# Optimization experiments

Hardware: AMD Instinct MI355X
Metric: run time of the kernel (lower is better)

Reference implementation:

```python
import jax, jax.numpy as jnp
import numpy as np

DIM = 512
HEADS = 4
HEAD_DIM = DIM // HEADS
HIDDEN = DIM * 2
DEPTH = 4
N = 32768
T = 4  # fixed branch/token dim


def _layernorm(x, w, b, eps=1e-5):
    m = jnp.mean(x, axis=-1, keepdims=True)
    v = jnp.mean(jnp.square(x - m), axis=-1, keepdims=True)
    return (x - m) * jax.lax.rsqrt(v + eps) * w + b


def setup_inputs() -> dict:
    key = jax.random.key(0)
    ks = jax.random.split(key, 24)
    s = 0.02
    d = {
        'x': jax.random.normal(ks[0], (N, DIM, T), dtype=jnp.float32),
        'branch_embed': s * jax.random.normal(ks[1], (T, DIM), dtype=jnp.float32),
        'ln1_w': jnp.ones((DEPTH, DIM), jnp.float32),
        'ln1_b': jnp.zeros((DEPTH, DIM), jnp.float32),
        'qkv_w': s * jax.random.normal(ks[2], (DEPTH, 3 * DIM, DIM), dtype=jnp.float32),
        'qkv_b': jnp.zeros((DEPTH, 3 * DIM), jnp.float32),
        'proj_w': s * jax.random.normal(ks[3], (DEPTH, DIM, DIM), dtype=jnp.float32),
        'proj_b': jnp.zeros((DEPTH, DIM), jnp.float32),
        'ln2_w': jnp.ones((DEPTH, DIM), jnp.float32),
        'ln2_b': jnp.zeros((DEPTH, DIM), jnp.float32),
        'ffn_w1': s * jax.random.normal(ks[4], (DEPTH, HIDDEN, DIM), dtype=jnp.float32),
        'ffn_b1': jnp.zeros((DEPTH, HIDDEN), jnp.float32),
        'ffn_w2': s * jax.random.normal(ks[5], (DEPTH, DIM, HIDDEN), dtype=jnp.float32),
        'ffn_b2': jnp.zeros((DEPTH, DIM), jnp.float32),
        'pool_q': s * jax.random.normal(ks[6], (DIM,), dtype=jnp.float32),
        'pool_w': s * jax.random.normal(ks[7], (DIM, DIM), dtype=jnp.float32),
        'out_ln_w': jnp.ones((DIM,), jnp.float32),
        'out_ln_b': jnp.zeros((DIM,), jnp.float32),
        'out_w1': s * jax.random.normal(ks[8], (DIM // 2, DIM), dtype=jnp.float32),
        'out_b1': jnp.zeros((DIM // 2,), jnp.float32),
        'out_w2': s * jax.random.normal(ks[9], (1, DIM // 2), dtype=jnp.float32),
        'out_b2': jnp.zeros((1,), jnp.float32),
    }
    return d


def reference(x, branch_embed, ln1_w, ln1_b, qkv_w, qkv_b, proj_w, proj_b,
              ln2_w, ln2_b, ffn_w1, ffn_b1, ffn_w2, ffn_b2,
              pool_q, pool_w, out_ln_w, out_ln_b, out_w1, out_b1, out_w2, out_b2):
    # (N, C, 4) -> (N, 4, C), add branch embedding
    x = jnp.swapaxes(x, 1, 2) + branch_embed[None]
    n = x.shape[0]
    scale = 1.0 / np.sqrt(HEAD_DIM)
    for i in range(DEPTH):
        # --- MHSA (pre-LN, eval mode -> dropout off) ---
        h = _layernorm(x, ln1_w[i], ln1_b[i])
        qkv = jnp.einsum('ntd,ed->nte', h, qkv_w[i]) + qkv_b[i]  # (N, T, 3D)
        q, k, v = jnp.split(qkv, 3, axis=-1)
        q = q.reshape(n, T, HEADS, HEAD_DIM).transpose(0, 2, 1, 3)
        k = k.reshape(n, T, HEADS, HEAD_DIM).transpose(0, 2, 1, 3)
        v = v.reshape(n, T, HEADS, HEAD_DIM).transpose(0, 2, 1, 3)
        scores = jnp.einsum('nhqd,nhkd->nhqk', q, k) * scale
        attn = jax.nn.softmax(scores, axis=-1)
        o = jnp.einsum('nhqk,nhkd->nhqd', attn, v)
        o = o.transpose(0, 2, 1, 3).reshape(n, T, DIM)
        o = jnp.einsum('ntd,ed->nte', o, proj_w[i]) + proj_b[i]
        x = x + o
        # --- FFN ---
        h = _layernorm(x, ln2_w[i], ln2_b[i])
        f = jax.nn.gelu(jnp.einsum('ntd,hd->nth', h, ffn_w1[i]) + ffn_b1[i], approximate=False)
        f = jnp.einsum('nth,dh->ntd', f, ffn_w2[i]) + ffn_b2[i]
        x = x + f
    # --- attention pooling head ---
    k = jnp.einsum('ntd,ed->nte', x, pool_w)            # pool_proj (no bias)
    score = jax.nn.softmax(jnp.einsum('d,ntd->nt', pool_q, k) / np.sqrt(DIM), axis=-1)
    z = jnp.einsum('nt,ntd->nd', score, x)
    z = _layernorm(z, out_ln_w, out_ln_b)
    z = jax.nn.gelu(z @ out_w1.T + out_b1, approximate=False)
    y = (z @ out_w2.T + out_b2)[:, 0]
    return y
```

## Files before the change

kernel.cpp:

```cpp
#include <hip/hip_runtime.h>

typedef unsigned short u16;
typedef unsigned int u32;
typedef __attribute__((ext_vector_type(8))) short s16x8;
typedef __attribute__((ext_vector_type(8))) unsigned short u16x8;
typedef __attribute__((ext_vector_type(4))) float f32x4;

__device__ __forceinline__ u16 f2bf(float f) {
    u32 u = __float_as_uint(f);
    u32 r = (u + 0x7fffu + ((u >> 16) & 1u)) >> 16;
    return (u16)r;
}
__device__ __forceinline__ float bf2f(u16 u) { return __uint_as_float(((u32)u) << 16); }
__device__ __forceinline__ float bflo(u32 u) { return __uint_as_float(u << 16); }
__device__ __forceinline__ float bfhi(u32 u) { return __uint_as_float(u & 0xffff0000u); }
__device__ __forceinline__ float gelu_exact(float v) {
    return 0.5f * v * (1.0f + erff(v * 0.70710678118654752f));
}

__device__ __forceinline__ void gload16(const void* g, void* l) {
    __builtin_amdgcn_global_load_lds(
        (const __attribute__((address_space(1))) u32*)g,
        (__attribute__((address_space(3))) u32*)l, 16, 0, 0);
}

__global__ void k_cvt(const float* __restrict__ in, u16* __restrict__ out, int n4) {
    int i = blockIdx.x * 256 + threadIdx.x;
    if (i < n4) {
        float4 v = *(const float4*)(in + (size_t)i * 4);
        u16 o0 = f2bf(v.x), o1 = f2bf(v.y), o2 = f2bf(v.z), o3 = f2bf(v.w);
        u32 lo = (u32)o0 | ((u32)o1 << 16);
        u32 hi = (u32)o2 | ((u32)o3 << 16);
        uint2 o; o.x = lo; o.y = hi;
        *(uint2*)(out + (size_t)i * 4) = o;
    }
}

__global__ __launch_bounds__(256) void k_embed_ln(const float* __restrict__ x,
                                                  const float* __restrict__ be,
                                                  const float* __restrict__ w,
                                                  const float* __restrict__ b,
                                                  u16* __restrict__ Xb,
                                                  u16* __restrict__ Hb) {
    __shared__ u16 ld[4][512];
    int s = blockIdx.x;
    int tid = threadIdx.x;
    const float* xs = x + (size_t)s * 2048;
#pragma unroll
    for (int i = 0; i < 2; ++i) {
        int d = tid + i * 256;
        float4 v = *(const float4*)(xs + d * 4);
        ld[0][d] = f2bf(v.x + be[d]);
        ld[1][d] = f2bf(v.y + be[512 + d]);
        ld[2][d] = f2bf(v.z + be[1024 + d]);
        ld[3][d] = f2bf(v.w + be[1536 + d]);
    }
    __syncthreads();
    int t = tid >> 6, lane = tid & 63;
    u16x8 raw = *(const u16x8*)(&ld[t][lane * 8]);
    *(u16x8*)(Xb + ((size_t)s * 4 + t) * 512 + lane * 8) = raw;
    float a[8];
#pragma unroll
    for (int j = 0; j < 8; ++j) a[j] = bf2f(raw[j]);
    float s1 = 0.f, s2 = 0.f;
#pragma unroll
    for (int j = 0; j < 8; ++j) { s1 += a[j]; s2 += a[j] * a[j]; }
#pragma unroll
    for (int d = 1; d < 64; d <<= 1) { s1 += __shfl_xor(s1, d); s2 += __shfl_xor(s2, d); }
    float mean = s1 * (1.0f / 512.0f);
    float var  = s2 * (1.0f / 512.0f) - mean * mean;
    float rstd = rsqrtf(var + 1e-5f);
    float4 w0 = *(const float4*)(w + lane * 8);
    float4 w1 = *(const float4*)(w + lane * 8 + 4);
    float4 b0 = *(const float4*)(b + lane * 8);
    float4 b1 = *(const float4*)(b + lane * 8 + 4);
    float wv[8] = {w0.x, w0.y, w0.z, w0.w, w1.x, w1.y, w1.z, w1.w};
    float bv[8] = {b0.x, b0.y, b0.z, b0.w, b1.x, b1.y, b1.z, b1.w};
    u16x8 o;
#pragma unroll
    for (int j = 0; j < 8; ++j) o[j] = f2bf((a[j] - mean) * rstd * wv[j] + bv[j]);
    *(u16x8*)(Hb + ((size_t)s * 4 + t) * 512 + lane * 8) = o;
}

__global__ __launch_bounds__(256) void k_ln(const u16* __restrict__ Xb,
                                            const float* __restrict__ w,
                                            const float* __restrict__ b,
                                            u16* __restrict__ H) {
    int row = blockIdx.x * 4 + (threadIdx.x >> 6);
    int lane = threadIdx.x & 63;
    u16x8 xv = *(const u16x8*)(Xb + (size_t)row * 512 + lane * 8);
    float a[8];
#pragma unroll
    for (int j = 0; j < 8; ++j) a[j] = bf2f(xv[j]);
    float s1 = 0.f, s2 = 0.f;
#pragma unroll
    for (int j = 0; j < 8; ++j) { s1 += a[j]; s2 += a[j] * a[j]; }
#pragma unroll
    for (int d = 1; d < 64; d <<= 1) { s1 += __shfl_xor(s1, d); s2 += __shfl_xor(s2, d); }
    float mean = s1 * (1.0f / 512.0f);
    float var  = s2 * (1.0f / 512.0f) - mean * mean;
    float rstd = rsqrtf(var + 1e-5f);
    float4 w0 = *(const float4*)(w + lane * 8);
    float4 w1 = *(const float4*)(w + lane * 8 + 4);
    float4 b0 = *(const float4*)(b + lane * 8);
    float4 b1 = *(const float4*)(b + lane * 8 + 4);
    float wv[8] = {w0.x, w0.y, w0.z, w0.w, w1.x, w1.y, w1.z, w1.w};
    float bv[8] = {b0.x, b0.y, b0.z, b0.w, b1.x, b1.y, b1.z, b1.w};
    u16x8 o;
#pragma unroll
    for (int j = 0; j < 8; ++j) o[j] = f2bf((a[j] - mean) * rstd * wv[j] + bv[j]);
    *(u16x8*)(H + (size_t)row * 512 + lane * 8) = o;
}

template <bool BIAS, bool GELU_, bool RESID>
__global__ __launch_bounds__(512, 2) void k_gemm256(const u16* __restrict__ A,
                                                    const u16* __restrict__ W,
                                                    const float* __restrict__ bias,
                                                    u16* __restrict__ Cb,
                                                    u16* __restrict__ Xbres,
                                                    int K, int ncols, int TN, int T) {
    __shared__ __align__(16) u16 lds[2 * 32768];
    int tid = threadIdx.x;
    int lane = tid & 63;
    int wid = tid >> 6;
    int G = gridDim.x, b = blockIdx.x;
    int start, end, step;
    if ((G & 7) == 0) {
        int xcd = b & 7, nxb = G >> 3, j = b >> 3;
        start = (int)(((long long)xcd * T) >> 3) + j;
        end   = (int)(((long long)(xcd + 1) * T) >> 3);
        step  = nxb;
    } else {
        start = (int)(((long long)b * T) / G);
        end   = (int)(((long long)(b + 1) * T) / G);
        step  = 1;
    }
    if (start >= end) return;
    int NS = K >> 6;
    int mgrp = wid >> 2, ngrp = wid & 3;

    f32x4 acc[8][4];
#pragma unroll
    for (int i = 0; i < 8; ++i)
#pragma unroll
        for (int j = 0; j < 4; ++j) acc[i][j] = (f32x4){0.f, 0.f, 0.f, 0.f};

    int srow = tid >> 3;
    int sel  = (((tid & 7) * 16) ^ ((srow & 7) << 4)) >> 1;
    size_t K64 = (size_t)K * 64;
    char* ldsB = (char*)lds;
    int wdst = wid * 1024;

    const u16 *cA0, *cA1, *cB0, *cB1, *nA0, *nA1, *nB0, *nB1;
    int cm0, cn0, nm0, nn0;
    auto tilePtrs = [&](int ti, const u16*& a0, const u16*& a1,
                        const u16*& b0, const u16*& b1, int& m0o, int& n0o) {
        int bx = ti / TN, by = ti - bx * TN;
        int m0 = bx * 256, n0 = by * 256;
        a0 = A + (size_t)(m0 + srow) * K + sel;
        a1 = A + (size_t)(m0 + 128 + srow) * K + sel;
        b0 = W + (size_t)(n0 + srow) * K + sel;
        b1 = W + (size_t)(n0 + 128 + srow) * K + sel;
        m0o = m0; n0o = n0;
    };

    auto S_Aq12 = [&](const u16* a0, const u16* a1, int s) {
        char* d = ldsB + (s & 1) * 65536 + wdst;
        gload16(a0 + (size_t)s * 64, d);
        gload16(a1 + (size_t)s * 64, d + 16384);
    };
    auto S_Aq34 = [&](const u16* a0, const u16* a1, int s) {
        char* d = ldsB + (s & 1) * 65536 + 8192 + wdst;
        gload16(a0 + K64 + (size_t)s * 64, d);
        gload16(a1 + K64 + (size_t)s * 64, d + 16384);
    };
    auto S_Blo = [&](const u16* b0, int s) {
        char* d = ldsB + (s & 1) * 65536 + 32768 + wdst;
        gload16(b0 + (size_t)s * 64, d);
        gload16(b0 + K64 + (size_t)s * 64, d + 8192);
    };
    auto S_Bhi = [&](const u16* b1, int s) {
        char* d = ldsB + (s & 1) * 65536 + 49152 + wdst;
        gload16(b1 + (size_t)s * 64, d);
        gload16(b1 + K64 + (size_t)s * 64, d + 8192);
    };

    int arow = mgrp * 128 + (lane & 15);
    int brow = ngrp * 64 + (lane & 15);
    int sub = (lane >> 4) << 4;
    int amask = ((arow & 7) << 4), bmask = ((brow & 7) << 4);
    int aoff0 = arow * 128 + (sub ^ amask);
    int boff0 = 32768 + brow * 128 + (sub ^ bmask);
    int aoff1 = arow * 128 + ((sub | 64) ^ amask);
    int boff1 = 32768 + brow * 128 + ((sub | 64) ^ bmask);

    tilePtrs(start, cA0, cA1, cB0, cB1, cm0, cn0);
    S_Blo(cB0, 0); S_Bhi(cB1, 0); S_Aq12(cA0, cA1, 0); S_Aq34(cA0, cA1, 0);
    S_Blo(cB0, 1); S_Bhi(cB1, 1); S_Aq12(cA0, cA1, 1);
    asm volatile("s_waitcnt vmcnt(6)" ::: "memory");
    __builtin_amdgcn_s_barrier();

    for (int ti = start; ti < end; ti += step) {
        bool hasNext = (ti + step < end);
        if (hasNext) tilePtrs(ti + step, nA0, nA1, nB0, nB1, nm0, nn0);

        s16x8 bfr[4][2];
        for (int s = 0; s < NS; ++s) {
            const char* sb = ldsB + (s & 1) * 65536;
            int st = s + 1, st2 = s + 2;
            bool n1 = st < NS, n2 = st2 < NS;
            s16x8 af[2][2];
#pragma unroll
            for (int ni = 0; ni < 4; ++ni) {
                bfr[ni][0] = *(const s16x8*)(sb + boff0 + ni * 2048);
                bfr[ni][1] = *(const s16x8*)(sb + boff1 + ni * 2048);
            }
            af[0][0] = *(const s16x8*)(sb + aoff0);
            af[0][1] = *(const s16x8*)(sb + aoff1);
            af[1][0] = *(const s16x8*)(sb + aoff0 + 2048);
            af[1][1] = *(const s16x8*)(sb + aoff1 + 2048);
            if (n1) S_Aq34(cA0, cA1, st); else if (hasNext) S_Aq34(nA0, nA1, st - NS);
            __builtin_amdgcn_s_barrier();
            __builtin_amdgcn_s_setprio(1);
#pragma unroll
            for (int mj = 0; mj < 2; ++mj)
#pragma unroll
                for (int ni = 0; ni < 4; ++ni) {
                    acc[mj][ni] = __builtin_amdgcn_mfma_f32_16x16x32_bf16(bfr[ni][0], af[mj][0], acc[mj][ni], 0, 0, 0);
                    acc[mj][ni] = __builtin_amdgcn_mfma_f32_16x16x32_bf16(bfr[ni][1], af[mj][1], acc[mj][ni], 0, 0, 0);
                }
            __builtin_amdgcn_s_setprio(0);
            __builtin_amdgcn_s_barrier();
#pragma unroll
            for (int mj = 0; mj < 2; ++mj) {
                af[mj][0] = *(const s16x8*)(sb + aoff0 + (2 + mj) * 2048);
                af[mj][1] = *(const s16x8*)(sb + aoff1 + (2 + mj) * 2048);
            }
            if (n2) S_Blo(cB0, st2); else if (hasNext) S_Blo(nB0, st2 - NS);
            __builtin_amdgcn_s_barrier();
            __builtin_amdgcn_s_setprio(1);
#pragma unroll
            for (int mj = 0; mj < 2; ++mj)
#pragma unroll
                for (int ni = 0; ni < 4; ++ni) {
                    acc[2 + mj][ni] = __builtin_amdgcn_mfma_f32_16x16x32_bf16(bfr[ni][0], af[mj][0], acc[2 + mj][ni], 0, 0, 0);
                    acc[2 + mj][ni] = __builtin_amdgcn_mfma_f32_16x16x32_bf16(bfr[ni][1], af[mj][1], acc[2 + mj][ni], 0, 0, 0);
                }
            __builtin_amdgcn_s_setprio(0);
            __builtin_amdgcn_s_barrier();
#pragma unroll
            for (int mj = 0; mj < 2; ++mj) {
                af[mj][0] = *(const s16x8*)(sb + aoff0 + (4 + mj) * 2048);
                af[mj][1] = *(const s16x8*)(sb + aoff1 + (4 + mj) * 2048);
            }
            if (n2) S_Bhi(cB1, st2); else if (hasNext) S_Bhi(nB1, st2 - NS);
            __builtin_amdgcn_s_barrier();
            __builtin_amdgcn_s_setprio(1);
#pragma unroll
            for (int mj = 0; mj < 2; ++mj)
#pragma unroll
                for (int ni = 0; ni < 4; ++ni) {
                    acc[4 + mj][ni] = __builtin_amdgcn_mfma_f32_16x16x32_bf16(bfr[ni][0], af[mj][0], acc[4 + mj][ni], 0, 0, 0);
                    acc[4 + mj][ni] = __builtin_amdgcn_mfma_f32_16x16x32_bf16(bfr[ni][1], af[mj][1], acc[4 + mj][ni], 0, 0, 0);
                }
            __builtin_amdgcn_s_setprio(0);
            __builtin_amdgcn_s_barrier();
#pragma unroll
            for (int mj = 0; mj < 2; ++mj) {
                af[mj][0] = *(const s16x8*)(sb + aoff0 + (6 + mj) * 2048);
                af[mj][1] = *(const s16x8*)(sb + aoff1 + (6 + mj) * 2048);
            }
            if (n2) S_Aq12(cA0, cA1, st2); else if (hasNext) S_Aq12(nA0, nA1, st2 - NS);
            __builtin_amdgcn_s_barrier();
            __builtin_amdgcn_s_setprio(1);
#pragma unroll
            for (int mj = 0; mj < 2; ++mj)
#pragma unroll
                for (int ni = 0; ni < 4; ++ni) {
                    acc[6 + mj][ni] = __builtin_amdgcn_mfma_f32_16x16x32_bf16(bfr[ni][0], af[mj][0], acc[6 + mj][ni], 0, 0, 0);
                    acc[6 + mj][ni] = __builtin_amdgcn_mfma_f32_16x16x32_bf16(bfr[ni][1], af[mj][1], acc[6 + mj][ni], 0, 0, 0);
                }
            __builtin_amdgcn_s_setprio(0);
            bool staged24 = n2 || hasNext;
            bool last = (s == NS - 1) && !hasNext;
            if (!last) {
                if (staged24) asm volatile("s_waitcnt vmcnt(6)" ::: "memory");
                else          asm volatile("s_waitcnt vmcnt(0)" ::: "memory");
                __builtin_amdgcn_s_barrier();
            }
        }

        int r_lane = lane & 15, cg = lane >> 4;
#pragma unroll
        for (int mi = 0; mi < 8; ++mi) {
            int row = cm0 + mgrp * 128 + mi * 16 + r_lane;
#pragma unroll
            for (int ni = 0; ni < 4; ++ni) {
                int c = cn0 + ngrp * 64 + ni * 16 + cg * 4;
                f32x4 v = acc[mi][ni];
                if (BIAS) {
                    float4 bb = *(const float4*)(bias + c);
                    v[0] += bb.x; v[1] += bb.y; v[2] += bb.z; v[3] += bb.w;
                }
                if (GELU_) {
#pragma unroll
                    for (int j = 0; j < 4; ++j) v[j] = gelu_exact(v[j]);
                }
                if (RESID) {
                    u16* px = Xbres + (size_t)row * 512 + c;
                    uint2 xv = *(uint2*)px;
                    float x0 = bflo(xv.x) + v[0];
                    float x1 = bfhi(xv.x) + v[1];
                    float x2 = bflo(xv.y) + v[2];
                    float x3 = bfhi(xv.y) + v[3];
                    uint2 o;
                    o.x = (u32)f2bf(x0) | ((u32)f2bf(x1) << 16);
                    o.y = (u32)f2bf(x2) | ((u32)f2bf(x3) << 16);
                    *(uint2*)px = o;
                } else {
                    u32 lo = (u32)f2bf(v[0]) | ((u32)f2bf(v[1]) << 16);
                    u32 hi = (u32)f2bf(v[2]) | ((u32)f2bf(v[3]) << 16);
                    uint2 o; o.x = lo; o.y = hi;
                    *(uint2*)(Cb + (size_t)row * ncols + c) = o;
                }
                acc[mi][ni] = (f32x4){0.f, 0.f, 0.f, 0.f};
            }
        }
        cA0 = nA0; cA1 = nA1; cB0 = nB0; cB1 = nB1; cm0 = nm0; cn0 = nn0;
    }
}

__global__ __launch_bounds__(256) void k_attn(const u16* __restrict__ QKV, u16* __restrict__ O) {
    int task = blockIdx.x * 4 + (threadIdx.x >> 6);
    int lane = threadIdx.x & 63;
    int s = task >> 2, h = task & 3;
    const u16* base = QKV + (size_t)s * 4 * 1536 + h * 128;
    float q[4][2], k[4][2], v[4][2];
#pragma unroll
    for (int t = 0; t < 4; ++t) {
        const u16* row = base + t * 1536;
        u32 uq = *(const u32*)(row + lane * 2);
        u32 uk = *(const u32*)(row + 512 + lane * 2);
        u32 uv = *(const u32*)(row + 1024 + lane * 2);
        q[t][0] = bflo(uq); q[t][1] = bfhi(uq);
        k[t][0] = bflo(uk); k[t][1] = bfhi(uk);
        v[t][0] = bflo(uv); v[t][1] = bfhi(uv);
    }
    float sc[4][4];
#pragma unroll
    for (int i = 0; i < 4; ++i)
#pragma unroll
        for (int j = 0; j < 4; ++j) {
            float p = q[i][0] * k[j][0] + q[i][1] * k[j][1];
#pragma unroll
            for (int d = 1; d < 64; d <<= 1) p += __shfl_xor(p, d);
            sc[i][j] = p * 0.08838834764831845f;
        }
    float o[4][2];
#pragma unroll
    for (int i = 0; i < 4; ++i) {
        float mx = fmaxf(fmaxf(sc[i][0], sc[i][1]), fmaxf(sc[i][2], sc[i][3]));
        float e0 = expf(sc[i][0] - mx), e1 = expf(sc[i][1] - mx);
        float e2 = expf(sc[i][2] - mx), e3 = expf(sc[i][3] - mx);
        float inv = 1.0f / (e0 + e1 + e2 + e3);
        float a0 = e0 * inv, a1 = e1 * inv, a2 = e2 * inv, a3 = e3 * inv;
        o[i][0] = a0 * v[0][0] + a1 * v[1][0] + a2 * v[2][0] + a3 * v[3][0];
        o[i][1] = a0 * v[0][1] + a1 * v[1][1] + a2 * v[2][1] + a3 * v[3][1];
    }
#pragma unroll
    for (int i = 0; i < 4; ++i) {
        u32 pk = (u32)f2bf(o[i][0]) | ((u32)f2bf(o[i][1]) << 16);
        *(u32*)(O + ((size_t)s * 4 + i) * 512 + h * 128 + lane * 2) = pk;
    }
}

__global__ __launch_bounds__(256) void k_pool(const u16* __restrict__ Xb, const u16* __restrict__ Kp,
                                              const float* __restrict__ pq,
                                              const float* __restrict__ olnw, const float* __restrict__ olnb,
                                              u16* __restrict__ Zb) {
    int s = blockIdx.x * 4 + (threadIdx.x >> 6);
    int lane = threadIdx.x & 63;
    float4 p0 = *(const float4*)(pq + lane * 8);
    float4 p1 = *(const float4*)(pq + lane * 8 + 4);
    float pqv[8] = {p0.x, p0.y, p0.z, p0.w, p1.x, p1.y, p1.z, p1.w};
    float dot[4];
#pragma unroll
    for (int t = 0; t < 4; ++t) {
        u16x8 kv = *(const u16x8*)(Kp + ((size_t)s * 4 + t) * 512 + lane * 8);
        float p = 0.f;
#pragma unroll
        for (int j = 0; j < 8; ++j) p += pqv[j] * bf2f(kv[j]);
#pragma unroll
        for (int d = 1; d < 64; d <<= 1) p += __shfl_xor(p, d);
        dot[t] = p * 0.044194173824159216f;
    }
    float mx = fmaxf(fmaxf(dot[0], dot[1]), fmaxf(dot[2], dot[3]));
    float e[4], se = 0.f;
#pragma unroll
    for (int t = 0; t < 4; ++t) { e[t] = expf(dot[t] - mx); se += e[t]; }
    float inv = 1.0f / se;
    float z[8] = {0, 0, 0, 0, 0, 0, 0, 0};
#pragma unroll
    for (int t = 0; t < 4; ++t) {
        float scv = e[t] * inv;
        u16x8 xv = *(const u16x8*)(Xb + ((size_t)s * 4 + t) * 512 + lane * 8);
#pragma unroll
        for (int j = 0; j < 8; ++j) z[j] += scv * bf2f(xv[j]);
    }
    float s1 = 0.f, s2 = 0.f;
#pragma unroll
    for (int j = 0; j < 8; ++j) { s1 += z[j]; s2 += z[j] * z[j]; }
#pragma unroll
    for (int d = 1; d < 64; d <<= 1) { s1 += __shfl_xor(s1, d); s2 += __shfl_xor(s2, d); }
    float mean = s1 * (1.0f / 512.0f);
    float var  = s2 * (1.0f / 512.0f) - mean * mean;
    float rstd = rsqrtf(var + 1e-5f);
    float4 w0 = *(const float4*)(olnw + lane * 8);
    float4 w1 = *(const float4*)(olnw + lane * 8 + 4);
    float4 b0 = *(const float4*)(olnb + lane * 8);
    float4 b1 = *(const float4*)(olnb + lane * 8 + 4);
    float wv[8] = {w0.x, w0.y, w0.z, w0.w, w1.x, w1.y, w1.z, w1.w};
    float bv[8] = {b0.x, b0.y, b0.z, b0.w, b1.x, b1.y, b1.z, b1.w};
    u16x8 o;
#pragma unroll
    for (int j = 0; j < 8; ++j) o[j] = f2bf((z[j] - mean) * rstd * wv[j] + bv[j]);
    *(u16x8*)(Zb + (size_t)s * 512 + lane * 8) = o;
}

__global__ __launch_bounds__(256) void k_out2(const u16* __restrict__ G, const float* __restrict__ w2,
                                              const float* __restrict__ b2, float* __restrict__ y) {
    int s = blockIdx.x * 4 + (threadIdx.x >> 6);
    int lane = threadIdx.x & 63;
    uint2 u = *(const uint2*)(G + (size_t)s * 256 + lane * 4);
    float4 wv = *(const float4*)(w2 + lane * 4);
    float p = bflo(u.x) * wv.x + bfhi(u.x) * wv.y + bflo(u.y) * wv.z + bfhi(u.y) * wv.w;
#pragma unroll
    for (int d = 1; d < 64; d <<= 1) p += __shfl_xor(p, d);
    if (lane == 0) y[s] = p + b2[0];
}

extern "C" void kernel_launch(void* const* d_in, const int* in_sizes, int n_in,
                              void* d_out, int out_size, void* d_ws, size_t ws_size,
                              hipStream_t stream) {
    const float* x     = (const float*)d_in[0];
    const float* be    = (const float*)d_in[1];
    const float* ln1w  = (const float*)d_in[2];
    const float* ln1b  = (const float*)d_in[3];
    const float* qkvw  = (const float*)d_in[4];
    const float* qkvb  = (const float*)d_in[5];
    const float* projw = (const float*)d_in[6];
    const float* projb = (const float*)d_in[7];
    const float* ln2w  = (const float*)d_in[8];
    const float* ln2b  = (const float*)d_in[9];
    const float* f1w   = (const float*)d_in[10];
    const float* f1b   = (const float*)d_in[11];
    const float* f2w   = (const float*)d_in[12];
    const float* f2b   = (const float*)d_in[13];
    const float* poolq = (const float*)d_in[14];
    const float* poolw = (const float*)d_in[15];
    const float* olnw  = (const float*)d_in[16];
    const float* olnb  = (const float*)d_in[17];
    const float* ow1   = (const float*)d_in[18];
    const float* ob1   = (const float*)d_in[19];
    const float* ow2   = (const float*)d_in[20];
    const float* ob2   = (const float*)d_in[21];
    float* y = (float*)d_out;

    int N = in_sizes[0] / 2048;

    char* p = (char*)d_ws;
    auto take = [&](size_t b) { char* r = p; p += (b + 255) & ~(size_t)255; return r; };
    u16* qkvWb  = (u16*)take((size_t)3145728 * 2);
    u16* projWb = (u16*)take((size_t)1048576 * 2);
    u16* f1Wb   = (u16*)take((size_t)2097152 * 2);
    u16* f2Wb   = (u16*)take((size_t)2097152 * 2);
    u16* poolWb = (u16*)take((size_t)262144 * 2);
    u16* ow1b   = (u16*)take((size_t)131072 * 2);
    size_t fixedB = (size_t)(p - (char*)d_ws);

    int S = N;
    while (S > 256 && fixedB + (size_t)S * 20480 + 65536 > ws_size) S >>= 1;
    int R = S * 4;
    int TM = R / 256;

    u16* Xb    = (u16*)take((size_t)R * 512 * 2);
    u16* Hb    = (u16*)take((size_t)R * 512 * 2);
    u16* QKVb  = (u16*)take((size_t)R * 1536 * 2);
    u16* Kpb = QKVb;
    u16* Fb  = QKVb;
    u16* Gb  = (u16*)((char*)QKVb + (size_t)R * 512 * 2);
    u16* Zb  = Hb;

    auto cvt = [&](const float* in, u16* out, int n) {
        int n4 = n / 4;
        k_cvt<<<(n4 + 255) / 256, 256, 0, stream>>>(in, out, n4);
    };
    cvt(qkvw, qkvWb, 3145728);
    cvt(projw, projWb, 1048576);
    cvt(f1w, f1Wb, 2097152);
    cvt(f2w, f2Wb, 2097152);
    cvt(poolw, poolWb, 262144);
    cvt(ow1, ow1b, 131072);

    auto gridFor = [](int T) { return T < 256 ? T : 256; };

    for (int c0 = 0; c0 < N; c0 += S) {
        const float* xin = x + (size_t)c0 * 2048;
        k_embed_ln<<<S, 256, 0, stream>>>(xin, be, ln1w, ln1b, Xb, Hb);
        for (int l = 0; l < 4; ++l) {
            if (l > 0)
                k_ln<<<R / 4, 256, 0, stream>>>(Xb, ln1w + l * 512, ln1b + l * 512, Hb);
            { int T = TM * 6;
              k_gemm256<true, false, false><<<gridFor(T), 512, 0, stream>>>(
                  Hb, qkvWb + (size_t)l * 786432, qkvb + l * 1536, QKVb, nullptr, 512, 1536, 6, T); }
            k_attn<<<S, 256, 0, stream>>>(QKVb, Hb);
            { int T = TM * 2;
              k_gemm256<true, false, true><<<gridFor(T), 512, 0, stream>>>(
                  Hb, projWb + (size_t)l * 262144, projb + l * 512, nullptr, Xb, 512, 512, 2, T); }
            k_ln<<<R / 4, 256, 0, stream>>>(Xb, ln2w + l * 512, ln2b + l * 512, Hb);
            { int T = TM * 4;
              k_gemm256<true, true, false><<<gridFor(T), 512, 0, stream>>>(
                  Hb, f1Wb + (size_t)l * 524288, f1b + l * 1024, Fb, nullptr, 512, 1024, 4, T); }
            { int T = TM * 2;
              k_gemm256<true, false, true><<<gridFor(T), 512, 0, stream>>>(
                  Fb, f2Wb + (size_t)l * 524288, f2b + l * 512, nullptr, Xb, 1024, 512, 2, T); }
        }
        { int T = TM * 2;
          k_gemm256<false, false, false><<<gridFor(T), 512, 0, stream>>>(
              Xb, poolWb, nullptr, Kpb, nullptr, 512, 512, 2, T); }
        k_pool<<<S / 4, 256, 0, stream>>>(Xb, Kpb, poolq, olnw, olnb, Zb);
        { int T = S / 256;
          k_gemm256<true, true, false><<<gridFor(T), 512, 0, stream>>>(
              Zb, ow1b, ob1, Gb, nullptr, 512, 256, 1, T); }
        k_out2<<<S / 4, 256, 0, stream>>>(Gb, ow2, ob2, y + c0);
    }
    (void)n_in; (void)out_size; (void)ws_size;
}
```

Before: 4.431 ms.

## Replace 256x256 GEMM with 128x128 tile, triple-buffered K=32 pipeline

Rewrites the persistent GEMM kernel from 256x256 tiles with 512 threads and two 64-wide K stages to 128x128 tiles with 256 threads, a 32-wide K step and a three-buffer LDS ring. The launch grid is raised to 768 blocks and occupancy is targeted at three blocks per CU. The aim is more parallelism, better load balance and fewer barriers per K step. The costs are lower arithmetic intensity per tile, more global traffic for the operands, and the loss of the XOR swizzle in LDS, which may cause bank conflicts.

```diff
diff --git a/kernel.cpp b/kernel.cpp
--- a/kernel.cpp
+++ b/kernel.cpp
@@ -113,13 +113,13 @@
 }
 
 template <bool BIAS, bool GELU_, bool RESID>
-__global__ __launch_bounds__(512, 2) void k_gemm256(const u16* __restrict__ A,
+__global__ __launch_bounds__(256, 3) void k_gemm128(const u16* __restrict__ A,
                                                     const u16* __restrict__ W,
                                                     const float* __restrict__ bias,
                                                     u16* __restrict__ Cb,
                                                     u16* __restrict__ Xbres,
                                                     int K, int ncols, int TN, int T) {
-    __shared__ __align__(16) u16 lds[2 * 32768];
+    __shared__ __align__(16) u16 lds[3 * 8192];
     int tid = threadIdx.x;
     int lane = tid & 63;
     int wid = tid >> 6;
@@ -136,164 +136,82 @@
         step  = 1;
     }
     if (start >= end) return;
-    int NS = K >> 6;
-    int mgrp = wid >> 2, ngrp = wid & 3;
-
-    f32x4 acc[8][4];
-#pragma unroll
-    for (int i = 0; i < 8; ++i)
+    int NS = K >> 5;
+    int mgrp = wid >> 1, ngrp = wid & 1;
+
+    f32x4 acc[4][4];
+#pragma unroll
+    for (int i = 0; i < 4; ++i)
 #pragma unroll
         for (int j = 0; j < 4; ++j) acc[i][j] = (f32x4){0.f, 0.f, 0.f, 0.f};
 
-    int srow = tid >> 3;
-    int sel  = (((tid & 7) * 16) ^ ((srow & 7) << 4)) >> 1;
-    size_t K64 = (size_t)K * 64;
+    int srow = tid >> 2;
+    int sel  = (tid & 3) * 8;
     char* ldsB = (char*)lds;
     int wdst = wid * 1024;
-
-    const u16 *cA0, *cA1, *cB0, *cB1, *nA0, *nA1, *nB0, *nB1;
+    size_t ROW64 = (size_t)K * 64;
+
+    const u16 *cA, *cB, *nA, *nB;
     int cm0, cn0, nm0, nn0;
-    auto tilePtrs = [&](int ti, const u16*& a0, const u16*& a1,
-                        const u16*& b0, const u16*& b1, int& m0o, int& n0o) {
+    auto tilePtrs = [&](int ti, const u16*& a, const u16*& w2, int& m0o, int& n0o) {
         int bx = ti / TN, by = ti - bx * TN;
-        int m0 = bx * 256, n0 = by * 256;
-        a0 = A + (size_t)(m0 + srow) * K + sel;
-        a1 = A + (size_t)(m0 + 128 + srow) * K + sel;
-        b0 = W + (size_t)(n0 + srow) * K + sel;
-        b1 = W + (size_t)(n0 + 128 + srow) * K + sel;
+        int m0 = bx * 128, n0 = by * 128;
+        a  = A + (size_t)(m0 + srow) * K + sel;
+        w2 = W + (size_t)(n0 + srow) * K + sel;
         m0o = m0; n0o = n0;
     };
-
-    auto S_Aq12 = [&](const u16* a0, const u16* a1, int s) {
-        char* d = ldsB + (s & 1) * 65536 + wdst;
-        gload16(a0 + (size_t)s * 64, d);
-        gload16(a1 + (size_t)s * 64, d + 16384);
+    auto STAGE = [&](const u16* a, const u16* w2, int s, int buf) {
+        char* d = ldsB + buf * 16384 + wdst;
+        const u16* ap = a + (size_t)s * 32;
+        const u16* bp = w2 + (size_t)s * 32;
+        gload16(ap, d);
+        gload16(ap + ROW64, d + 4096);
+        gload16(bp, d + 8192);
+        gload16(bp + ROW64, d + 12288);
     };
-    auto S_Aq34 = [&](const u16* a0, const u16* a1, int s) {
-        char* d = ldsB + (s & 1) * 65536 + 8192 + wdst;
-        gload16(a0 + K64 + (size_t)s * 64, d);
-        gload16(a1 + K64 + (size_t)s * 64, d + 16384);
-    };
-    auto S_Blo = [&](const u16* b0, int s) {
-        char* d = ldsB + (s & 1) * 65536 + 32768 + wdst;
-        gload16(b0 + (size_t)s * 64, d);
-        gload16(b0 + K64 + (size_t)s * 64, d + 8192);
-    };
-    auto S_Bhi = [&](const u16* b1, int s) {
-        char* d = ldsB + (s & 1) * 65536 + 49152 + wdst;
-        gload16(b1 + (size_t)s * 64, d);
-        gload16(b1 + K64 + (size_t)s * 64, d + 8192);
-    };
-
-    int arow = mgrp * 128 + (lane & 15);
-    int brow = ngrp * 64 + (lane & 15);
-    int sub = (lane >> 4) << 4;
-    int amask = ((arow & 7) << 4), bmask = ((brow & 7) << 4);
-    int aoff0 = arow * 128 + (sub ^ amask);
-    int boff0 = 32768 + brow * 128 + (sub ^ bmask);
-    int aoff1 = arow * 128 + ((sub | 64) ^ amask);
-    int boff1 = 32768 + brow * 128 + ((sub | 64) ^ bmask);
-
-    tilePtrs(start, cA0, cA1, cB0, cB1, cm0, cn0);
-    S_Blo(cB0, 0); S_Bhi(cB1, 0); S_Aq12(cA0, cA1, 0); S_Aq34(cA0, cA1, 0);
-    S_Blo(cB0, 1); S_Bhi(cB1, 1); S_Aq12(cA0, cA1, 1);
-    asm volatile("s_waitcnt vmcnt(6)" ::: "memory");
-    __builtin_amdgcn_s_barrier();
+
+    int aoff = (mgrp * 64 + (lane & 15)) * 64 + (lane >> 4) * 16;
+    int boff = 8192 + (ngrp * 64 + (lane & 15)) * 64 + (lane >> 4) * 16;
+
+    tilePtrs(start, cA, cB, cm0, cn0);
+    STAGE(cA, cB, 0, 0);
+    STAGE(cA, cB, 1, 1);
+    int bufc = 0;
 
     for (int ti = start; ti < end; ti += step) {
-        bool hasNext = (ti + step < end);
-        if (hasNext) tilePtrs(ti + step, nA0, nA1, nB0, nB1, nm0, nn0);
-
-        s16x8 bfr[4][2];
+        bool hasNext = (ti + step) < end;
+        if (hasNext) tilePtrs(ti + step, nA, nB, nm0, nn0);
+
         for (int s = 0; s < NS; ++s) {
-            const char* sb = ldsB + (s & 1) * 65536;
-            int st = s + 1, st2 = s + 2;
-            bool n1 = st < NS, n2 = st2 < NS;
-            s16x8 af[2][2];
-#pragma unroll
-            for (int ni = 0; ni < 4; ++ni) {
-                bfr[ni][0] = *(const s16x8*)(sb + boff0 + ni * 2048);
-                bfr[ni][1] = *(const s16x8*)(sb + boff1 + ni * 2048);
-            }
-            af[0][0] = *(const s16x8*)(sb + aoff0);
-            af[0][1] = *(const s16x8*)(sb + aoff1);
-            af[1][0] = *(const s16x8*)(sb + aoff0 + 2048);
-            af[1][1] = *(const s16x8*)(sb + aoff1 + 2048);
-            if (n1) S_Aq34(cA0, cA1, st); else if (hasNext) S_Aq34(nA0, nA1, st - NS);
+            if (s == NS - 1 && !hasNext)
+                asm volatile("s_waitcnt vmcnt(0)" ::: "memory");
+            else
+                asm volatile("s_waitcnt vmcnt(4)" ::: "memory");
             __builtin_amdgcn_s_barrier();
+            const char* sb = ldsB + bufc * 16384;
+            s16x8 af[4], bf[4];
+#pragma unroll
+            for (int mi = 0; mi < 4; ++mi) af[mi] = *(const s16x8*)(sb + aoff + mi * 1024);
+#pragma unroll
+            for (int ni = 0; ni < 4; ++ni) bf[ni] = *(const s16x8*)(sb + boff + ni * 1024);
+            int b2 = bufc + 2; if (b2 >= 3) b2 -= 3;
+            int st2 = s + 2;
+            if (st2 < NS) STAGE(cA, cB, st2, b2);
+            else if (hasNext) STAGE(nA, nB, st2 - NS, b2);
             __builtin_amdgcn_s_setprio(1);
 #pragma unroll
-            for (int mj = 0; mj < 2; ++mj)
-#pragma unroll
-                for (int ni = 0; ni < 4; ++ni) {
-                    acc[mj][ni] = __builtin_amdgcn_mfma_f32_16x16x32_bf16(bfr[ni][0], af[mj][0], acc[mj][ni], 0, 0, 0);
-                    acc[mj][ni] = __builtin_amdgcn_mfma_f32_16x16x32_bf16(bfr[ni][1], af[mj][1], acc[mj][ni], 0, 0, 0);
-                }
+            for (int mi = 0; mi < 4; ++mi)
+#pragma unroll
+                for (int ni = 0; ni < 4; ++ni)
+                    acc[mi][ni] = __builtin_amdgcn_mfma_f32_16x16x32_bf16(bf[ni], af[mi], acc[mi][ni], 0, 0, 0);
             __builtin_amdgcn_s_setprio(0);
-            __builtin_amdgcn_s_barrier();
-#pragma unroll
-            for (int mj = 0; mj < 2; ++mj) {
-                af[mj][0] = *(const s16x8*)(sb + aoff0 + (2 + mj) * 2048);
-                af[mj][1] = *(const s16x8*)(sb + aoff1 + (2 + mj) * 2048);
-            }
-            if (n2) S_Blo(cB0, st2); else if (hasNext) S_Blo(nB0, st2 - NS);
-            __builtin_amdgcn_s_barrier();
-            __builtin_amdgcn_s_setprio(1);
-#pragma unroll
-            for (int mj = 0; mj < 2; ++mj)
-#pragma unroll
-                for (int ni = 0; ni < 4; ++ni) {
-                    acc[2 + mj][ni] = __builtin_amdgcn_mfma_f32_16x16x32_bf16(bfr[ni][0], af[mj][0], acc[2 + mj][ni], 0, 0, 0);
-                    acc[2 + mj][ni] = __builtin_amdgcn_mfma_f32_16x16x32_bf16(bfr[ni][1], af[mj][1], acc[2 + mj][ni], 0, 0, 0);
-                }
-            __builtin_amdgcn_s_setprio(0);
-            __builtin_amdgcn_s_barrier();
-#pragma unroll
-            for (int mj = 0; mj < 2; ++mj) {
-                af[mj][0] = *(const s16x8*)(sb + aoff0 + (4 + mj) * 2048);
-                af[mj][1] = *(const s16x8*)(sb + aoff1 + (4 + mj) * 2048);
-            }
-            if (n2) S_Bhi(cB1, st2); else if (hasNext) S_Bhi(nB1, st2 - NS);
-            __builtin_amdgcn_s_barrier();
-            __builtin_amdgcn_s_setprio(1);
-#pragma unroll
-            for (int mj = 0; mj < 2; ++mj)
-#pragma unroll
-                for (int ni = 0; ni < 4; ++ni) {
-                    acc[4 + mj][ni] = __builtin_amdgcn_mfma_f32_16x16x32_bf16(bfr[ni][0], af[mj][0], acc[4 + mj][ni], 0, 0, 0);
-                    acc[4 + mj][ni] = __builtin_amdgcn_mfma_f32_16x16x32_bf16(bfr[ni][1], af[mj][1], acc[4 + mj][ni], 0, 0, 0);
-                }
-            __builtin_amdgcn_s_setprio(0);
-            __builtin_amdgcn_s_barrier();
-#pragma unroll
-            for (int mj = 0; mj < 2; ++mj) {
-                af[mj][0] = *(const s16x8*)(sb + aoff0 + (6 + mj) * 2048);
-                af[mj][1] = *(const s16x8*)(sb + aoff1 + (6 + mj) * 2048);
-            }
-            if (n2) S_Aq12(cA0, cA1, st2); else if (hasNext) S_Aq12(nA0, nA1, st2 - NS);
-            __builtin_amdgcn_s_barrier();
-            __builtin_amdgcn_s_setprio(1);
-#pragma unroll
-            for (int mj = 0; mj < 2; ++mj)
-#pragma unroll
-                for (int ni = 0; ni < 4; ++ni) {
-                    acc[6 + mj][ni] = __builtin_amdgcn_mfma_f32_16x16x32_bf16(bfr[ni][0], af[mj][0], acc[6 + mj][ni], 0, 0, 0);
-                    acc[6 + mj][ni] = __builtin_amdgcn_mfma_f32_16x16x32_bf16(bfr[ni][1], af[mj][1], acc[6 + mj][ni], 0, 0, 0);
-                }
-            __builtin_amdgcn_s_setprio(0);
-            bool staged24 = n2 || hasNext;
-            bool last = (s == NS - 1) && !hasNext;
-            if (!last) {
-                if (staged24) asm volatile("s_waitcnt vmcnt(6)" ::: "memory");
-                else          asm volatile("s_waitcnt vmcnt(0)" ::: "memory");
-                __builtin_amdgcn_s_barrier();
-            }
+            bufc = bufc + 1; if (bufc >= 3) bufc -= 3;
         }
 
         int r_lane = lane & 15, cg = lane >> 4;
 #pragma unroll
-        for (int mi = 0; mi < 8; ++mi) {
-            int row = cm0 + mgrp * 128 + mi * 16 + r_lane;
+        for (int mi = 0; mi < 4; ++mi) {
+            int row = cm0 + mgrp * 64 + mi * 16 + r_lane;
 #pragma unroll
             for (int ni = 0; ni < 4; ++ni) {
                 int c = cn0 + ngrp * 64 + ni * 16 + cg * 4;
@@ -326,7 +244,7 @@
                 acc[mi][ni] = (f32x4){0.f, 0.f, 0.f, 0.f};
             }
         }
-        cA0 = nA0; cA1 = nA1; cB0 = nB0; cB1 = nB1; cm0 = nm0; cn0 = nn0;
+        cA = nA; cB = nB; cm0 = nm0; cn0 = nn0;
     }
 }
 
@@ -481,7 +399,7 @@
     int S = N;
     while (S > 256 && fixedB + (size_t)S * 20480 + 65536 > ws_size) S >>= 1;
     int R = S * 4;
-    int TM = R / 256;
+    int TM = R / 128;
 
     u16* Xb    = (u16*)take((size_t)R * 512 * 2);
     u16* Hb    = (u16*)take((size_t)R * 512 * 2);
@@ -502,7 +420,7 @@
     cvt(poolw, poolWb, 262144);
     cvt(ow1, ow1b, 131072);
 
-    auto gridFor = [](int T) { return T < 256 ? T : 256; };
+    auto gridFor = [](int T) { return T < 768 ? T : 768; };
 
     for (int c0 = 0; c0 < N; c0 += S) {
         const float* xin = x + (size_t)c0 * 2048;
@@ -510,28 +428,28 @@
         for (int l = 0; l < 4; ++l) {
             if (l > 0)
                 k_ln<<<R / 4, 256, 0, stream>>>(Xb, ln1w + l * 512, ln1b + l * 512, Hb);
-            { int T = TM * 6;
-              k_gemm256<true, false, false><<<gridFor(T), 512, 0, stream>>>(
-                  Hb, qkvWb + (size_t)l * 786432, qkvb + l * 1536, QKVb, nullptr, 512, 1536, 6, T); }
+            { int T = TM * 12;
+              k_gemm128<true, false, false><<<gridFor(T), 256, 0, stream>>>(
+                  Hb, qkvWb + (size_t)l * 786432, qkvb + l * 1536, QKVb, nullptr, 512, 1536, 12, T); }
             k_attn<<<S, 256, 0, stream>>>(QKVb, Hb);
-            { int T = TM * 2;
-              k_gemm256<true, false, true><<<gridFor(T), 512, 0, stream>>>(
-                  Hb, projWb + (size_t)l * 262144, projb + l * 512, nullptr, Xb, 512, 512, 2, T); }
+            { int T = TM * 4;
+              k_gemm128<true, false, true><<<gridFor(T), 256, 0, stream>>>(
+                  Hb, projWb + (size_t)l * 262144, projb + l * 512, nullptr, Xb, 512, 512, 4, T); }
             k_ln<<<R / 4, 256, 0, stream>>>(Xb, ln2w + l * 512, ln2b + l * 512, Hb);
+            { int T = TM * 8;
+              k_gemm128<true, true, false><<<gridFor(T), 256, 0, stream>>>(
+                  Hb, f1Wb + (size_t)l * 524288, f1b + l * 1024, Fb, nullptr, 512, 1024, 8, T); }
             { int T = TM * 4;
-              k_gemm256<true, true, false><<<gridFor(T), 512, 0, stream>>>(
-                  Hb, f1Wb + (size_t)l * 524288, f1b + l * 1024, Fb, nullptr, 512, 1024, 4, T); }
-            { int T = TM * 2;
-              k_gemm256<true, false, true><<<gridFor(T), 512, 0, stream>>>(
-                  Fb, f2Wb + (size_t)l * 524288, f2b + l * 512, nullptr, Xb, 1024, 512, 2, T); }
+              k_gemm128<true, false, true><<<gridFor(T), 256, 0, stream>>>(
+                  Fb, f2Wb + (size_t)l * 524288, f2b + l * 512, nullptr, Xb, 1024, 512, 4, T); }
         }
-        { int T = TM * 2;
-          k_gemm256<false, false, false><<<gridFor(T), 512, 0, stream>>>(
-              Xb, poolWb, nullptr, Kpb, nullptr, 512, 512, 2, T); }
+        { int T = TM * 4;
+          k_gemm128<false, false, false><<<gridFor(T), 256, 0, stream>>>(
+              Xb, poolWb, nullptr, Kpb, nullptr, 512, 512, 4, T); }
         k_pool<<<S / 4, 256, 0, stream>>>(Xb, Kpb, poolq, olnw, olnb, Zb);
-        { int T = S / 256;
-          k_gemm256<true, true, false><<<gridFor(T), 512, 0, stream>>>(
-              Zb, ow1b, ob1, Gb, nullptr, 512, 256, 1, T); }
+        { int T = (S / 128) * 2;
+          k_gemm128<true, true, false><<<gridFor(T), 256, 0, stream>>>(
+              Zb, ow1b, ob1, Gb, nullptr, 512, 256, 2, T); }
         k_out2<<<S / 4, 256, 0, stream>>>(Gb, ow2, ob2, y + c0);
     }
     (void)n_in; (void)out_size; (void)ws_size;
```

New measurement: 4.919 ms. 11.0% more time.
